# Performance work log

Measured on AMD Instinct MI355X. Metric: run time of the kernel, lower is better.

## Reference

```python
import jax, jax.numpy as jnp
import numpy as np

B, T, C, H, D = 2, 2048, 1024, 16, 64


def setup_inputs() -> dict:
    key = jax.random.key(0)
    k1, k2, k3, k4, k5 = jax.random.split(key, 5)
    x = jax.random.normal(k1, (B, T, C), dtype=jnp.float32)
    Wq = jax.random.normal(k2, (H, C, D), dtype=jnp.float32) * 0.02
    Wk = jax.random.normal(k3, (H, C, D), dtype=jnp.float32) * 0.02
    Wv = jax.random.normal(k4, (H, C, D), dtype=jnp.float32) * 0.02
    Wo = jax.random.normal(k5, (C, C), dtype=jnp.float32) * 0.02
    bo = jnp.zeros((C,), dtype=jnp.float32)
    return {"x": x, "Wq": Wq, "Wk": Wk, "Wv": Wv, "Wo": Wo, "bo": bo}


def reference(x, Wq, Wk, Wv, Wo, bo):
    # per-head projections (batched over heads instead of a python loop)
    q = jnp.einsum('btc,hcd->bhtd', x, Wq)
    k = jnp.einsum('btc,hcd->bhtd', x, Wk)
    v = jnp.einsum('btc,hcd->bhtd', x, Wv)
    scale = jnp.asarray(D, x.dtype) ** -0.5
    wei = jnp.einsum('bhtd,bhsd->bhts', q, k) * scale  # [B,H,T,T]
    causal = jnp.tril(jnp.ones((T, T), dtype=bool))
    wei = jnp.where(causal, wei, jnp.asarray(-jnp.inf, wei.dtype))
    attn = jax.nn.softmax(wei, axis=-1)
    out = jnp.einsum('bhts,bhsd->bhtd', attn, v)  # [B,H,T,D]
    # concat heads (head order h0..hH-1 along feature dim)
    out = out.transpose(0, 2, 1, 3).reshape(B, T, C)
    # output projection: nn.Linear -> y = x @ W^T + b  (dropout p=0 is identity)
    return out @ Wo.T + bo
```

## Files before the change

### kernel.cpp

```cpp
#include <hip/hip_runtime.h>
#include <hip/hip_bf16.h>
#include <cstdint>
#include <math.h>

#define B_DIM 2
#define T_SEQ 2048
#define C_DIM 1024
#define H_NUM 16
#define D_HEAD 64
#define M_ROWS (B_DIM * T_SEQ)
#define N_QKV (3 * H_NUM * D_HEAD)

using short8  = __attribute__((ext_vector_type(8))) short;
using short4v = __attribute__((ext_vector_type(4))) short;
using f32x4   = __attribute__((ext_vector_type(4))) float;

__device__ __forceinline__ short f2bf(float f) {
  union { __hip_bfloat16 h; short s; } u;
  u.h = __float2bfloat16(f);
  return u.s;
}
__device__ __forceinline__ short f2bf_trunc(float f) {
  union { float f; unsigned u; } v;
  v.f = f;
  return (short)(v.u >> 16);
}

__device__ __forceinline__ void gld_lds16(short* lds, const short* g) {
  __builtin_amdgcn_global_load_lds(
      (const unsigned int __attribute__((address_space(1)))*)g,
      (unsigned int __attribute__((address_space(3)))*)lds, 16, 0, 0);
}

#define BAR_VM(N)                                                    \
  do {                                                               \
    asm volatile("s_waitcnt vmcnt(" #N ") lgkmcnt(0)" ::: "memory"); \
    __builtin_amdgcn_s_barrier();                                    \
    __builtin_amdgcn_sched_barrier(0);                               \
  } while (0)

__global__ __launch_bounds__(256) void cvt_f32_bf16(const float* __restrict__ in,
                                                    short* __restrict__ out, int n8) {
  int i = blockIdx.x * 256 + threadIdx.x;
  if (i >= n8) return;
  const float4* p = reinterpret_cast<const float4*>(in) + (size_t)i * 2;
  float4 a = p[0], b = p[1];
  short8 o;
  o[0] = f2bf(a.x); o[1] = f2bf(a.y); o[2] = f2bf(a.z); o[3] = f2bf(a.w);
  o[4] = f2bf(b.x); o[5] = f2bf(b.y); o[6] = f2bf(b.z); o[7] = f2bf(b.w);
  reinterpret_cast<short8*>(out)[i] = o;
}

__global__ __launch_bounds__(256) void pack_w(const float* __restrict__ Wq,
                                              const float* __restrict__ Wk,
                                              const float* __restrict__ Wv,
                                              short* __restrict__ Wt) {
  int bid  = blockIdx.x;
  int proj = bid >> 8;
  int h    = (bid >> 4) & 15;
  int cb   = bid & 15;
  const float* W = (proj == 0) ? Wq : ((proj == 1) ? Wk : Wv);
  const float* src = W + ((size_t)h * C_DIM + (size_t)cb * 64) * D_HEAD;

  __shared__ float tile[64][65];
  int tid = threadIdx.x;

#pragma unroll
  for (int j = 0; j < 4; j++) {
    int flat = tid + j * 256;
    int c    = flat >> 4;
    int d4   = flat & 15;
    float4 v = reinterpret_cast<const float4*>(src + (size_t)c * D_HEAD)[d4];
    tile[c][d4 * 4 + 0] = v.x;
    tile[c][d4 * 4 + 1] = v.y;
    tile[c][d4 * 4 + 2] = v.z;
    tile[c][d4 * 4 + 3] = v.w;
  }
  __syncthreads();

  int d     = tid >> 2;
  int cpart = (tid & 3) * 16;
  short* dst = Wt + ((size_t)(proj * H_NUM + h) * D_HEAD + d) * C_DIM + cb * 64 + cpart;
  short8 o0, o1;
#pragma unroll
  for (int j = 0; j < 8; j++) {
    o0[j] = f2bf(tile[cpart + j][d]);
    o1[j] = f2bf(tile[cpart + 8 + j][d]);
  }
  *reinterpret_cast<short8*>(dst)     = o0;
  *reinterpret_cast<short8*>(dst + 8) = o1;
}

template <int MODE, int BMT>
__global__ __launch_bounds__(256) void gemm_bt(
    const short* __restrict__ A, const short* __restrict__ Bt,
    const float* __restrict__ bias,
    short* __restrict__ qb, short* __restrict__ kb, short* __restrict__ vtb,
    float* __restrict__ outb,
    int M, int N, int K) {
  constexpr int BK = 32;
  constexpr int MR = BMT / 32;
  constexpr int NLA = BMT / 64;
  __shared__ short As[3][BMT * BK];
  __shared__ short Bs[3][128 * BK];

  int tid  = threadIdx.x;
  int lane = tid & 63;
  int wv   = tid >> 6;
  int q15  = lane & 15, g = lane >> 4;
  int ntn  = N >> 7;
  int bm   = blockIdx.x / ntn;
  int bn   = blockIdx.x % ntn;
  int row0 = bm * BMT, col0 = bn << 7;
  int wm   = (wv >> 1) * (BMT / 2);
  int wn   = (wv & 1) << 6;

  f32x4 acc[MR][4];
#pragma unroll
  for (int i = 0; i < MR; i++)
#pragma unroll
    for (int j = 0; j < 4; j++) acc[i][j] = (f32x4){0.f, 0.f, 0.f, 0.f};

  const short* ag = A  + (size_t)(row0 + (tid >> 2)) * K + (tid & 3) * 8;
  const short* bg = Bt + (size_t)(col0 + (tid >> 2)) * K + (tid & 3) * 8;
  const size_t gstep = (size_t)64 * K;

  auto stage = [&](int ks, int buf) {
    const short* a  = ag + (size_t)ks * BK;
    const short* bb = bg + (size_t)ks * BK;
    gld_lds16(&As[buf][0] + tid * 8, a);
    if constexpr (NLA == 2) gld_lds16(&As[buf][64 * BK] + tid * 8, a + gstep);
    gld_lds16(&Bs[buf][0] + tid * 8, bb);
    gld_lds16(&Bs[buf][64 * BK] + tid * 8, bb + gstep);
  };

  int nk = K / BK;
  stage(0, 0);
  stage(1, 1);
  if constexpr (NLA == 2) {
    asm volatile("s_waitcnt vmcnt(4)" ::: "memory");
  } else {
    asm volatile("s_waitcnt vmcnt(3)" ::: "memory");
  }
  __builtin_amdgcn_s_barrier();
  __builtin_amdgcn_sched_barrier(0);

  for (int k = 0; k < nk; ++k) {
    int buf = k % 3;
    if (k + 2 < nk) stage(k + 2, (k + 2) % 3);

    short8 af[MR], bf[4];
#pragma unroll
    for (int mi = 0; mi < MR; mi++)
      af[mi] = *reinterpret_cast<const short8*>(
          &As[buf][(wm + mi * 16 + q15) * BK + g * 8]);
#pragma unroll
    for (int ni = 0; ni < 4; ni++)
      bf[ni] = *reinterpret_cast<const short8*>(
          &Bs[buf][(wn + ni * 16 + q15) * BK + g * 8]);
    __builtin_amdgcn_s_setprio(1);
#pragma unroll
    for (int mi = 0; mi < MR; mi++)
#pragma unroll
      for (int ni = 0; ni < 4; ni++)
        acc[mi][ni] = __builtin_amdgcn_mfma_f32_16x16x32_bf16(af[mi], bf[ni],
                                                              acc[mi][ni], 0, 0, 0);
    __builtin_amdgcn_s_setprio(0);

    if (k + 1 < nk) {
      if (k + 2 < nk) {
        if constexpr (NLA == 2) { BAR_VM(4); } else { BAR_VM(3); }
      } else {
        BAR_VM(0);
      }
    }
  }

#pragma unroll
  for (int mi = 0; mi < MR; mi++) {
#pragma unroll
    for (int ni = 0; ni < 4; ni++) {
      int rb  = row0 + wm + mi * 16 + (g << 2);
      int col = col0 + wn + ni * 16 + q15;
      f32x4 v = acc[mi][ni];
      if (MODE == 0) {
        int proj = col >> 10;
        int hh   = (col >> 6) & (H_NUM - 1);
        int d    = col & (D_HEAD - 1);
        int b    = rb >> 11;
        int t    = rb & (T_SEQ - 1);
        if (proj < 2) {
          float scl = (proj == 0) ? 0.125f : 1.0f;
          short* dst = (proj == 0 ? qb : kb) +
                       ((size_t)(b * H_NUM + hh) * T_SEQ) * D_HEAD + d;
#pragma unroll
          for (int r = 0; r < 4; r++)
            dst[(size_t)(t + r) * D_HEAD] = f2bf(v[r] * scl);
        } else {
          short4v pk;
#pragma unroll
          for (int r = 0; r < 4; r++) pk[r] = f2bf(v[r]);
          short* dst = vtb + ((size_t)(b * H_NUM + hh) * D_HEAD + d) * T_SEQ + t;
          *reinterpret_cast<short4v*>(dst) = pk;
        }
      } else {
        float bb = bias[col];
#pragma unroll
        for (int r = 0; r < 4; r++)
          outb[(size_t)(rb + r) * N + col] = v[r] + bb;
      }
    }
  }
}

__global__ __launch_bounds__(256, 4) void attn_fwd(const short* __restrict__ qg,
                                                   const short* __restrict__ kg,
                                                   const short* __restrict__ vt,
                                                   short* __restrict__ ob) {
  constexpr float LOG2E = 1.44269504f;
  int bid  = blockIdx.x;
  int q2   = bid >> 8;
  int r    = bid & 255;
  int bh   = (r & 7) * 4 + q2;
  int sb   = r >> 3;
  int strip = (q2 & 1) ? sb : 31 - sb;
  int b    = bh >> 4;
  int h    = bh & 15;
  int tid  = threadIdx.x, lane = tid & 63, wv = tid >> 6;
  int q15  = lane & 15, g = lane >> 4;
  int qr   = strip * 64 + wv * 16;

  __shared__ short arena[16384];

  const short* qp = qg + (size_t)bh * T_SEQ * D_HEAD;
  const short* kp = kg + (size_t)bh * T_SEQ * D_HEAD;
  const short* vp = vt + (size_t)bh * D_HEAD * T_SEQ;

  int r8    = lane >> 3;
  int gcb   = ((lane & 7) * 16) ^ (r8 << 4);
  int srow0 = wv * 16;

  int hh = (q15 & 7) << 4;
  int koff0 = ((0 * 64 + g * 16) ^ hh) >> 1;
  int koff1 = ((1 * 64 + g * 16) ^ hh) >> 1;
  int voff[4];
#pragma unroll
  for (int st = 0; st < 4; st++) voff[st] = ((st * 32 + g * 8) ^ hh) >> 1;

  short8 qf[2];
#pragma unroll
  for (int kk = 0; kk < 2; kk++)
    qf[kk] = *reinterpret_cast<const short8*>(
        qp + (size_t)(qr + q15) * D_HEAD + kk * 32 + g * 8);

  f32x4 acc[4];
#pragma unroll
  for (int dt = 0; dt < 4; dt++) acc[dt] = (f32x4){0.f, 0.f, 0.f, 0.f};
  float m_ = -1e30f, l_ = 0.f;

  int nch = strip + 1;

  auto stage = [&](int c, int pbuf) {
    const short* ks = kp + (size_t)(c * 64 + srow0 + r8) * D_HEAD + (gcb >> 1);
    const short* vs = vp + (size_t)(srow0 + r8) * T_SEQ + c * 64 + (gcb >> 1);
    short* kd = arena + pbuf * 4096 + srow0 * 64 + lane * 8;
    short* vd = arena + 8192 + pbuf * 4096 + srow0 * 64 + lane * 8;
    gld_lds16(kd, ks);
    gld_lds16(kd + 8 * 64, ks + (size_t)8 * D_HEAD);
    gld_lds16(vd, vs);
    gld_lds16(vd + 8 * 64, vs + (size_t)8 * T_SEQ);
  };

  stage(0, 0);
  BAR_VM(0);

  for (int c = 0; c < nch; ++c) {
    int s0 = c * 64;
    if (c + 1 < nch) stage(c + 1, (c + 1) & 1);
    const short* Kb = arena + (c & 1) * 4096;
    const short* Vb = arena + 8192 + (c & 1) * 4096;

    short8 kf[4][2];
#pragma unroll
    for (int st = 0; st < 4; st++) {
      int rbase = (st * 16 + q15) * 64;
      kf[st][0] = *reinterpret_cast<const short8*>(&Kb[rbase + koff0]);
      kf[st][1] = *reinterpret_cast<const short8*>(&Kb[rbase + koff1]);
    }

    f32x4 sv[4];
    __builtin_amdgcn_s_setprio(1);
#pragma unroll
    for (int st = 0; st < 4; st++) {
      f32x4 s = (f32x4){0.f, 0.f, 0.f, 0.f};
      s = __builtin_amdgcn_mfma_f32_16x16x32_bf16(kf[st][0], qf[0], s, 0, 0, 0);
      s = __builtin_amdgcn_mfma_f32_16x16x32_bf16(kf[st][1], qf[1], s, 0, 0, 0);
      sv[st] = s;
    }
    __builtin_amdgcn_s_setprio(0);

    short4v vf[4][4];
#pragma unroll
    for (int st = 0; st < 4; st++)
#pragma unroll
      for (int dt = 0; dt < 4; dt++)
        vf[st][dt] = *reinterpret_cast<const short4v*>(
            &Vb[(dt * 16 + q15) * 64 + voff[st]]);

    if (c == nch - 1) {
#pragma unroll
      for (int st = 0; st < 4; st++)
#pragma unroll
        for (int r2 = 0; r2 < 4; r2++) {
          int sg = s0 + st * 16 + g * 4 + r2;
          if (sg > qr + q15) sv[st][r2] = -1e30f;
        }
    }

    float mx = sv[0][0];
#pragma unroll
    for (int st = 0; st < 4; st++)
#pragma unroll
      for (int r2 = 0; r2 < 4; r2++) mx = fmaxf(mx, sv[st][r2]);
    mx = fmaxf(mx, __shfl_xor(mx, 16));
    mx = fmaxf(mx, __shfl_xor(mx, 32));
    if (!__all(mx <= m_ + 8.0f)) {
      float mnew = fmaxf(m_, mx);
      float sc   = __builtin_amdgcn_exp2f((m_ - mnew) * LOG2E);
      m_ = mnew;
      l_ *= sc;
#pragma unroll
      for (int dt = 0; dt < 4; dt++) acc[dt] *= sc;
    }
    float mcur = m_;
    short4v pbf[4];
    float ps = 0.f;
#pragma unroll
    for (int st = 0; st < 4; st++)
#pragma unroll
      for (int r2 = 0; r2 < 4; r2++) {
        float p = __builtin_amdgcn_exp2f((sv[st][r2] - mcur) * LOG2E);
        ps += p;
        pbf[st][r2] = f2bf_trunc(p);
      }
    ps += __shfl_xor(ps, 16);
    ps += __shfl_xor(ps, 32);
    l_ += ps;

    __builtin_amdgcn_s_setprio(1);
#pragma unroll
    for (int st = 0; st < 4; st++)
#pragma unroll
      for (int dt = 0; dt < 4; dt++) {
#if __has_builtin(__builtin_amdgcn_mfma_f32_16x16x16bf16_1k)
        acc[dt] = __builtin_amdgcn_mfma_f32_16x16x16bf16_1k(
            vf[st][dt], pbf[st], acc[dt], 0, 0, 0);
#else
        short4v v4 = vf[st][dt];
        short4v p4 = pbf[st];
        short8 az = (short8){v4[0], v4[1], v4[2], v4[3], 0, 0, 0, 0};
        short8 bz = (short8){p4[0], p4[1], p4[2], p4[3], 0, 0, 0, 0};
        acc[dt] =
            __builtin_amdgcn_mfma_f32_16x16x32_bf16(az, bz, acc[dt], 0, 0, 0);
#endif
      }
    __builtin_amdgcn_s_setprio(0);

    BAR_VM(0);
  }

  short* OlW = arena + wv * (16 * 68);
  float inv = 1.0f / l_;
#pragma unroll
  for (int dt = 0; dt < 4; dt++)
#pragma unroll
    for (int r2 = 0; r2 < 4; r2++)
      OlW[q15 * 68 + dt * 16 + g * 4 + r2] = f2bf(acc[dt][r2] * inv);
  int row = lane >> 2, cb = (lane & 3) * 16;
  size_t base = ((size_t)(b * T_SEQ) + qr + row) * C_DIM + h * 64 + cb;
  const short* src = OlW + row * 68 + cb;
  *reinterpret_cast<short8*>(ob + base) = *reinterpret_cast<const short8*>(src);
  *reinterpret_cast<short8*>(ob + base + 8) =
      *reinterpret_cast<const short8*>(src + 8);
}

extern "C" void kernel_launch(void* const* d_in, const int* in_sizes, int n_in,
                              void* d_out, int out_size, void* d_ws, size_t ws_size,
                              hipStream_t stream) {
  const float* x  = (const float*)d_in[0];
  const float* Wq = (const float*)d_in[1];
  const float* Wk = (const float*)d_in[2];
  const float* Wv = (const float*)d_in[3];
  const float* Wo = (const float*)d_in[4];
  const float* bo = (const float*)d_in[5];
  float* out = (float*)d_out;

  char* ws = (char*)d_ws;
  short* xb   = (short*)(ws + 0);
  short* Wt   = (short*)(ws + 8388608);
  short* Wob  = (short*)(ws + 14680064);
  short* qb   = (short*)(ws + 16777216);
  short* kb   = (short*)(ws + 25165824);
  short* vtb  = (short*)(ws + 33554432);
  short* obuf = xb;

  cvt_f32_bf16<<<2048, 256, 0, stream>>>(x, xb, M_ROWS * C_DIM / 8);
  cvt_f32_bf16<<<512, 256, 0, stream>>>(Wo, Wob, C_DIM * C_DIM / 8);
  pack_w<<<768, 256, 0, stream>>>(Wq, Wk, Wv, Wt);

  gemm_bt<0, 128><<<(M_ROWS / 128) * (N_QKV / 128), 256, 0, stream>>>(
      xb, Wt, nullptr, qb, kb, vtb, nullptr, M_ROWS, N_QKV, C_DIM);

  attn_fwd<<<1024, 256, 0, stream>>>(qb, kb, vtb, obuf);

  gemm_bt<1, 64><<<(M_ROWS / 64) * (C_DIM / 128), 256, 0, stream>>>(
      obuf, Wob, bo, nullptr, nullptr, nullptr, out, M_ROWS, C_DIM, C_DIM);
}
```

Measured before the change: 119.1 us.

## Fold log2e into Q scale and compute softmax row sums with MFMA

```diff
diff --git a/kernel.cpp b/kernel.cpp
--- a/kernel.cpp
+++ b/kernel.cpp
@@ -20,10 +20,11 @@
   u.h = __float2bfloat16(f);
   return u.s;
 }
-__device__ __forceinline__ short f2bf_trunc(float f) {
-  union { float f; unsigned u; } v;
-  v.f = f;
-  return (short)(v.u >> 16);
+
+__device__ __forceinline__ unsigned pk2bf(float a, float b) {
+  union { float f; unsigned u; } ua, ub;
+  ua.f = a; ub.f = b;
+  return __builtin_amdgcn_perm(ub.u, ua.u, 0x07060302u);
 }
 
 __device__ __forceinline__ void gld_lds16(short* lds, const short* g) {
@@ -190,7 +191,7 @@
         int b    = rb >> 11;
         int t    = rb & (T_SEQ - 1);
         if (proj < 2) {
-          float scl = (proj == 0) ? 0.125f : 1.0f;
+          float scl = (proj == 0) ? 0.125f * 1.44269504f : 1.0f;
           short* dst = (proj == 0 ? qb : kb) +
                        ((size_t)(b * H_NUM + hh) * T_SEQ) * D_HEAD + d;
 #pragma unroll
@@ -217,7 +218,6 @@
                                                    const short* __restrict__ kg,
                                                    const short* __restrict__ vt,
                                                    short* __restrict__ ob) {
-  constexpr float LOG2E = 1.44269504f;
   int bid  = blockIdx.x;
   int q2   = bid >> 8;
   int r    = bid & 255;
@@ -256,7 +256,11 @@
   f32x4 acc[4];
 #pragma unroll
   for (int dt = 0; dt < 4; dt++) acc[dt] = (f32x4){0.f, 0.f, 0.f, 0.f};
-  float m_ = -1e30f, l_ = 0.f;
+  f32x4 lacc = (f32x4){0.f, 0.f, 0.f, 0.f};
+  float m_ = -1e30f;
+
+  const short4v ones4 = (short4v){(short)0x3F80, (short)0x3F80,
+                                  (short)0x3F80, (short)0x3F80};
 
   int nch = strip + 1;
 
@@ -317,60 +321,70 @@
         }
     }
 
-    float mx = sv[0][0];
-#pragma unroll
-    for (int st = 0; st < 4; st++)
-#pragma unroll
-      for (int r2 = 0; r2 < 4; r2++) mx = fmaxf(mx, sv[st][r2]);
+    float t0 = fmaxf(fmaxf(sv[0][0], sv[0][1]), sv[0][2]);
+    float t1 = fmaxf(fmaxf(sv[0][3], sv[1][0]), sv[1][1]);
+    float t2 = fmaxf(fmaxf(sv[1][2], sv[1][3]), sv[2][0]);
+    float t3 = fmaxf(fmaxf(sv[2][1], sv[2][2]), sv[2][3]);
+    float t4 = fmaxf(fmaxf(sv[3][0], sv[3][1]), sv[3][2]);
+    float mx = fmaxf(fmaxf(fmaxf(t0, t1), t2),
+                     fmaxf(fmaxf(t3, t4), sv[3][3]));
     mx = fmaxf(mx, __shfl_xor(mx, 16));
     mx = fmaxf(mx, __shfl_xor(mx, 32));
-    if (!__all(mx <= m_ + 8.0f)) {
+
+    if (!__all(mx <= m_ + 11.5f)) {
       float mnew = fmaxf(m_, mx);
-      float sc   = __builtin_amdgcn_exp2f((m_ - mnew) * LOG2E);
+      float sc   = __builtin_amdgcn_exp2f(m_ - mnew);
       m_ = mnew;
-      l_ *= sc;
+      lacc *= sc;
 #pragma unroll
       for (int dt = 0; dt < 4; dt++) acc[dt] *= sc;
     }
     float mcur = m_;
+
     short4v pbf[4];
-    float ps = 0.f;
-#pragma unroll
-    for (int st = 0; st < 4; st++)
-#pragma unroll
-      for (int r2 = 0; r2 < 4; r2++) {
-        float p = __builtin_amdgcn_exp2f((sv[st][r2] - mcur) * LOG2E);
-        ps += p;
-        pbf[st][r2] = f2bf_trunc(p);
-      }
-    ps += __shfl_xor(ps, 16);
-    ps += __shfl_xor(ps, 32);
-    l_ += ps;
+#pragma unroll
+    for (int st = 0; st < 4; st++) {
+      float p0 = __builtin_amdgcn_exp2f(sv[st][0] - mcur);
+      float p1 = __builtin_amdgcn_exp2f(sv[st][1] - mcur);
+      float p2 = __builtin_amdgcn_exp2f(sv[st][2] - mcur);
+      float p3 = __builtin_amdgcn_exp2f(sv[st][3] - mcur);
+      union { short4v s; unsigned u[2]; } P;
+      P.u[0] = pk2bf(p0, p1);
+      P.u[1] = pk2bf(p2, p3);
+      pbf[st] = P.s;
+    }
 
     __builtin_amdgcn_s_setprio(1);
 #pragma unroll
-    for (int st = 0; st < 4; st++)
-#pragma unroll
-      for (int dt = 0; dt < 4; dt++) {
+    for (int st = 0; st < 4; st++) {
 #if __has_builtin(__builtin_amdgcn_mfma_f32_16x16x16bf16_1k)
+      lacc = __builtin_amdgcn_mfma_f32_16x16x16bf16_1k(ones4, pbf[st], lacc, 0, 0, 0);
+#pragma unroll
+      for (int dt = 0; dt < 4; dt++)
         acc[dt] = __builtin_amdgcn_mfma_f32_16x16x16bf16_1k(
             vf[st][dt], pbf[st], acc[dt], 0, 0, 0);
 #else
+      short4v p4 = pbf[st];
+      short8 bz = (short8){p4[0], p4[1], p4[2], p4[3], 0, 0, 0, 0};
+      short8 oz = (short8){(short)0x3F80, (short)0x3F80, (short)0x3F80,
+                           (short)0x3F80, 0, 0, 0, 0};
+      lacc = __builtin_amdgcn_mfma_f32_16x16x32_bf16(oz, bz, lacc, 0, 0, 0);
+#pragma unroll
+      for (int dt = 0; dt < 4; dt++) {
         short4v v4 = vf[st][dt];
-        short4v p4 = pbf[st];
         short8 az = (short8){v4[0], v4[1], v4[2], v4[3], 0, 0, 0, 0};
-        short8 bz = (short8){p4[0], p4[1], p4[2], p4[3], 0, 0, 0, 0};
         acc[dt] =
             __builtin_amdgcn_mfma_f32_16x16x32_bf16(az, bz, acc[dt], 0, 0, 0);
+      }
 #endif
-      }
+    }
     __builtin_amdgcn_s_setprio(0);
 
     BAR_VM(0);
   }
 
   short* OlW = arena + wv * (16 * 68);
-  float inv = 1.0f / l_;
+  float inv = 1.0f / lacc[0];
 #pragma unroll
   for (int dt = 0; dt < 4; dt++)
 #pragma unroll
```

After: 115.2 us. -3.3%, faster.
